# Optimization experiments

Measured on AMD Instinct MI355X. Metric: run time of the kernel, lower is better.

Reference implementation:

```python
import jax, jax.numpy as jnp
import numpy as np

# ---- static config (mirrors init_kwargs) ----
N_DIM = 3                      # manifold dimension n
D_COMP = 6                     # n(n+1)/2 metric components
M_PER = (12, 12, 12)           # HSGP basis functions per dim
M_STAR = 12 * 12 * 12          # 1728
T_STEPS = 50                   # time points in linspace(0,1,t)
C_SCALE = 1.5                  # HSGP domain scaling c
BATCH = 8192
ROWS = np.array([0, 1, 1, 2, 2, 2])   # lower-tri fill order of metric components
COLS = np.array([0, 0, 1, 0, 1, 2])


def _phi_dphi(x, L):
    """HSGP eigenfunctions and their spatial derivatives.
    x: [B, 3], L: [3] -> phi [B, M_STAR], dphi [B, M_STAR, 3]."""
    s, c = [], []
    for d in range(N_DIM):
        k = jnp.arange(1, M_PER[d] + 1, dtype=x.dtype)
        w = jnp.pi * k / (2.0 * L[d])                      # [m_d] frequencies
        arg = w[None, :] * (x[:, d:d + 1] + L[d])          # [B, m_d]
        scale = 1.0 / jnp.sqrt(L[d])
        s.append(scale * jnp.sin(arg))
        c.append(scale * jnp.cos(arg) * w[None, :])
    B = x.shape[0]
    phi = jnp.einsum('bi,bj,bk->bijk', s[0], s[1], s[2]).reshape(B, -1)
    d0 = jnp.einsum('bi,bj,bk->bijk', c[0], s[1], s[2]).reshape(B, -1)
    d1 = jnp.einsum('bi,bj,bk->bijk', s[0], c[1], s[2]).reshape(B, -1)
    d2 = jnp.einsum('bi,bj,bk->bijk', s[0], s[1], c[2]).reshape(B, -1)
    return phi, jnp.stack([d0, d1, d2], axis=-1)


def _omega(L):
    """[M_STAR, 3] angular frequencies of the tensor-product basis."""
    ks = [jnp.arange(1, m + 1, dtype=L.dtype) for m in M_PER]
    kg = jnp.stack(jnp.meshgrid(*ks, indexing='ij'), axis=-1).reshape(-1, N_DIM)
    return jnp.pi * kg / (2.0 * L[None, :])


def _metric_and_grad(x, W, L):
    """Metric g [B,3,3] and its spatial derivative dg [B,3,3,3] (last axis = d/dx_r)."""
    phi, dphi = _phi_dphi(x, L)
    gf = phi @ W.T                                   # [B, 6]
    dgf = jnp.einsum('bmr,dm->bdr', dphi, W)         # [B, 6, 3]
    B = x.shape[0]
    eye = jnp.eye(N_DIM, dtype=x.dtype)
    gl = jnp.zeros((B, N_DIM, N_DIM), x.dtype).at[:, ROWS, COLS].set(gf)
    g = gl + jnp.swapaxes(gl, 1, 2) - gl * eye + eye   # symmetrize + identity offset
    dgl = jnp.zeros((B, N_DIM, N_DIM, N_DIM), x.dtype).at[:, ROWS, COLS, :].set(dgf)
    dg = dgl + jnp.swapaxes(dgl, 1, 2) - dgl * eye[None, :, :, None]
    return g, dg


def _acceleration(pos, vel, W, L):
    """Geodesic equation: a^k = -Gamma^k_{ij} v^i v^j."""
    g, dg = _metric_and_grad(pos, W, L)
    ginv = jnp.linalg.inv(g)
    t1 = jnp.swapaxes(dg, 2, 3)            # [b,l,i,j] = d_i g_{lj}
    t3 = jnp.transpose(dg, (0, 3, 1, 2))   # [b,l,i,j] = d_l g_{ij}
    gamma = 0.5 * jnp.einsum('bkl,blij->bkij', ginv, t1 + dg - t3)
    return -jnp.einsum('bkij,bi,bj->bk', gamma, vel, vel)


def _integrate(pos0, vel0, W, L):
    dt = 1.0 / (T_STEPS - 1)

    def f(p, v):
        return v, _acceleration(p, v, W, L)

    def step(carry, _):
        p, v = carry
        dp1, dv1 = f(p, v)
        dp2, dv2 = f(p + 0.5 * dt * dp1, v + 0.5 * dt * dv1)
        dp3, dv3 = f(p + 0.5 * dt * dp2, v + 0.5 * dt * dv2)
        dp4, dv4 = f(p + dt * dp3, v + dt * dv3)
        pn = p + (dt / 6.0) * (dp1 + 2 * dp2 + 2 * dp3 + dp4)
        vn = v + (dt / 6.0) * (dv1 + 2 * dv2 + 2 * dv3 + dv4)
        return (pn, vn), (pn, vn)

    _, (ps, vs) = jax.lax.scan(step, (pos0, vel0), None, length=T_STEPS - 1)
    pos_traj = jnp.concatenate([pos0[None], ps], axis=0)   # [T, B, 3]
    vel_traj = jnp.concatenate([vel0[None], vs], axis=0)
    return jnp.stack([pos_traj, vel_traj], axis=1)          # [T, 2, B, 3]


def setup_inputs() -> dict:
    key = jax.random.key(0)
    k1, k2, k3, k4, k5 = jax.random.split(key, 5)
    return {
        'pos0': jax.random.normal(k1, (BATCH, N_DIM), jnp.float32),
        'vel0': jax.random.normal(k2, (BATCH, N_DIM), jnp.float32),
        'beta': 0.02 * jax.random.normal(k3, (D_COMP, M_STAR), jnp.float32),
        'ls': 0.5 + jax.random.uniform(k4, (D_COMP, N_DIM), jnp.float32),
        'basis': jax.random.normal(k5, (256, N_DIM), jnp.float32),
    }


def reference(pos0, vel0, beta, ls, basis):
    # HSGP domain half-widths from the linearization anchor points
    L = C_SCALE * jnp.max(jnp.abs(basis), axis=0)           # [3]
    om2 = _omega(L) ** 2                                     # [M_STAR, 3]
    # ExpQuad sqrt spectral density per GP component
    sqrt_psd = ((2.0 * jnp.pi) ** (N_DIM / 4.0)) \
        * jnp.sqrt(jnp.prod(ls, axis=1, keepdims=True)) \
        * jnp.exp(-0.25 * jnp.einsum('mi,di->dm', om2, ls ** 2))  # [6, M_STAR]
    W = beta * sqrt_psd                                      # [6, M_STAR]
    return _integrate(pos0, vel0, W, L)
```

## Files before the change

kernel.cpp:

```cpp
#include <hip/hip_runtime.h>
#include <math.h>

#define BATCH  8192
#define TSTEPS 50
#define PTS    32
#define NTHR   768
#define KSTR   168
#define GKSTR  160
#define TABSTR 100
#define NROW   96
#define PI_F   3.14159265358979323846f

typedef __bf16 bf16x8 __attribute__((ext_vector_type(8)));
typedef float  f32x4  __attribute__((ext_vector_type(4)));

__device__ __forceinline__ unsigned pack2bf(float a, float b) {
    unsigned short ua = __builtin_bit_cast(unsigned short, (__bf16)a);
    unsigned short ub = __builtin_bit_cast(unsigned short, (__bf16)b);
    return (unsigned)ua | ((unsigned)ub << 16);
}

__global__ void precompute_kernel(const float* __restrict__ beta,
                                  const float* __restrict__ ls,
                                  const float* __restrict__ basis,
                                  unsigned short* __restrict__ Wb,
                                  float* __restrict__ auxg)
{
    __shared__ float red[256];
    __shared__ float Ls[3], W1s[3];
    int t = threadIdx.x;

    for (int d = 0; d < 3; ++d) {
        red[t] = fabsf(basis[t*3 + d]);
        __syncthreads();
        for (int s = 128; s > 0; s >>= 1) {
            if (t < s) red[t] = fmaxf(red[t], red[t+s]);
            __syncthreads();
        }
        if (t == 0) {
            float L = 1.5f * red[0];
            Ls[d]  = L;
            W1s[d] = PI_F / (2.0f * L);
        }
        __syncthreads();
    }

    float pref[6], l20[6], l21[6], l22[6];
    #pragma unroll
    for (int dd = 0; dd < 6; ++dd) {
        float a = ls[dd*3+0], b = ls[dd*3+1], c = ls[dd*3+2];
        pref[dd] = 3.9685803f * sqrtf(a*b*c);
        l20[dd] = a*a; l21[dd] = b*b; l22[dd] = c*c;
    }

    for (int idx = t; idx < 96*GKSTR; idx += 256) {
        int n = idx / GKSTR, k = idx - n*GKSTR;
        int d = n >> 4, i = n & 15;
        float v = 0.0f;
        if (i < 12 && k < 144) {
            int j = k / 12, kk = k - (k/12)*12;
            float o0 = W1s[0]*(float)(i+1);
            float o1 = W1s[1]*(float)(j+1);
            float o2 = W1s[2]*(float)(kk+1);
            float e = expf(-0.25f*(o0*o0*l20[d] + o1*o1*l21[d] + o2*o2*l22[d]));
            v = beta[d*1728 + i*144 + k] * pref[d] * e;
        }
        Wb[idx] = __builtin_bit_cast(unsigned short, (__bf16)v);
    }

    if (t < 3) {
        auxg[t]     = Ls[t];
        auxg[3 + t] = W1s[t];
        auxg[6 + t] = 1.0f / sqrtf(Ls[t]);
    }
}

__global__ void __launch_bounds__(NTHR) geodesic_kernel(
    const float* __restrict__ pos0, const float* __restrict__ vel0,
    const unsigned short* __restrict__ Wbg, const float* __restrict__ auxg,
    float* __restrict__ out)
{
    __shared__ __align__(16) __bf16 P[NROW*KSTR];
    __shared__ __align__(16) float tabs[2][PTS][TABSTR];
    __shared__ __align__(16) float scr[2][PTS][28];

    const int tid = threadIdx.x;

    for (int idx = tid; idx < NROW*KSTR/2; idx += NTHR) ((unsigned*)P)[idx] = 0u;
    for (int idx = tid; idx < 2*PTS*TABSTR; idx += NTHR) ((float*)tabs)[idx] = 0.f;

    const float L0 = auxg[0], L1 = auxg[1], L2 = auxg[2];
    const float w10 = auxg[3], w11 = auxg[4], w12 = auxg[5];
    const float isq0 = auxg[6], isq1 = auxg[7], isq2 = auxg[8];

    const int w = tid >> 6, lane = tid & 63;
    const int nt = w >> 1, mb = (w & 1) * 3;
    const int lrow = lane & 15, lkg = lane >> 4;
    const int nn = nt*16 + lrow;
    const int ptn = nn / 3, pn = nn - 3*ptn;

    bf16x8 wfrag[3][5];
    {
        const __bf16* Wb = (const __bf16*)Wbg;
        #pragma unroll
        for (int mt = 0; mt < 3; ++mt)
            #pragma unroll
            for (int ks = 0; ks < 5; ++ks)
                wfrag[mt][ks] = *(const bf16x8*)(Wb + ((mb+mt)*16 + lrow)*GKSTR + ks*32 + lkg*8);
    }

    const bool owner = (w < 4);
    const int  myp = (w << 3) + (lane & 7);
    const int  rep = lane >> 3;
    float px=0,py=0,pz=0, vx=0,vy=0,vz=0, vcx=0,vcy=0,vcz=0;
    float vsx=0,vsy=0,vsz=0, asx=0,asy=0,asz=0;
    float pnx=0,pny=0,pnz=0;
    float qnx=0,qny=0,qnz=0;
    size_t pg3 = 0;

    const float dt  = 1.0f/49.0f;
    const float hdt = 0.5f/49.0f;
    const float sdt = dt/6.0f;

    if (owner) {
        pg3 = (size_t)(blockIdx.x * PTS + myp) * 3u;
        px = pos0[pg3+0]; py = pos0[pg3+1]; pz = pos0[pg3+2];
        vx = vel0[pg3+0]; vy = vel0[pg3+1]; vz = vel0[pg3+2];
        vcx = vx; vcy = vy; vcz = vz;
        qnx = fmaf(hdt,vx,px); qny = fmaf(hdt,vy,py); qnz = fmaf(hdt,vz,pz);
        if (lane < 8) {
            out[pg3+0] = px; out[pg3+1] = py; out[pg3+2] = pz;
            out[(size_t)BATCH*3 + pg3 + 0] = vx;
            out[(size_t)BATCH*3 + pg3 + 1] = vy;
            out[(size_t)BATCH*3 + pg3 + 2] = vz;
        }
    }
    __syncthreads();

    if (owner) {
        float* tp = &tabs[0][myp][0];
        #pragma unroll 1
        for (int r = rep; r < 36; r += 8) {
            int d = (r>=24)?2:((r>=12)?1:0);
            int k = r - 12*d;
            float q   = (d==0)?px:((d==1)?py:pz);
            float Ld  = (d==0)?L0:((d==1)?L1:L2);
            float w1d = (d==0)?w10:((d==1)?w11:w12);
            float isd = (d==0)?isq0:((d==1)?isq1:isq2);
            float wk = w1d * (float)(k+1);
            float sn, cs;
            __sincosf(wk*(q + Ld), &sn, &cs);
            int offs = (d==0)?0:((d==1)?32:56);
            int offc = offs + ((d==0)?16:12);
            tp[offs+k] = isd*sn;
            tp[offc+k] = isd*cs*wk;
        }
    }
    __syncthreads();

    #pragma unroll 1
    for (int g = 0; g <= 196; ++g) {
        const int cb = g & 1;

        if (g < 196 && !owner) {
            int idx = (w-4)*64 + lane;
            #pragma unroll 1
            for (int rr = 0; rr < 2; ++rr) {
                int u = idx + rr*512;
                if (rr == 1 && idx >= 256) break;
                int pt = u / 24;
                int role = u - pt*24;
                int j = role >> 1, kb = (role & 1)*6;
                const float* tb = &tabs[cb][pt][0];
                float s1 = tb[32 + j], c1 = tb[44 + j];
                float2 sa = *(const float2*)&tb[56 + kb];
                float2 sb = *(const float2*)&tb[58 + kb];
                float2 sg = *(const float2*)&tb[60 + kb];
                float2 ca = *(const float2*)&tb[68 + kb];
                float2 cbv = *(const float2*)&tb[70 + kb];
                float2 cg = *(const float2*)&tb[72 + kb];
                float s2v[6] = {sa.x, sa.y, sb.x, sb.y, sg.x, sg.y};
                float c2v[6] = {ca.x, ca.y, cbv.x, cbv.y, cg.x, cg.y};
                int colb = j*12 + kb;
                unsigned* pss = (unsigned*)&P[(pt*3 + 0)*KSTR + colb];
                unsigned* pcs = (unsigned*)&P[(pt*3 + 1)*KSTR + colb];
                unsigned* psc = (unsigned*)&P[(pt*3 + 2)*KSTR + colb];
                #pragma unroll
                for (int u2 = 0; u2 < 3; ++u2) {
                    pss[u2] = pack2bf(s1*s2v[2*u2], s1*s2v[2*u2+1]);
                    pcs[u2] = pack2bf(c1*s2v[2*u2], c1*s2v[2*u2+1]);
                    psc[u2] = pack2bf(s1*c2v[2*u2], s1*c2v[2*u2+1]);
                }
            }
        }
        if (g > 0 && owner) {
            const int sp = (g-1) & 3;
            const f32x4* spr = (const f32x4*)&scr[cb^1][myp][0];
            f32x4 q0 = spr[0], q1 = spr[1], q2 = spr[2], q3 = spr[3], q4 = spr[4], q5 = spr[5];

            float ux = vcx, uy = vcy, uz = vcz;

            float g00 = q0[0]+1.f, g10 = q0[1], g11 = q0[2]+1.f;
            float g20 = q0[3], g21 = q1[0], g22 = q1[1]+1.f;
            float d0a0=q1[2], d0a1=q1[3], d0a2=q2[0], d0a3=q2[1], d0a4=q2[2], d0a5=q2[3];
            float d1a0=q3[0], d1a1=q3[1], d1a2=q3[2], d1a3=q3[3], d1a4=q4[0], d1a5=q4[1];
            float d2a0=q4[2], d2a1=q4[3], d2a2=q5[0], d2a3=q5[1], d2a4=q5[2], d2a5=q5[3];

            float a00 = g11*g22 - g21*g21;
            float a01 = g20*g21 - g10*g22;
            float a02 = g10*g21 - g20*g11;
            float a11 = g00*g22 - g20*g20;
            float a12 = g10*g20 - g00*g21;
            float a22 = g00*g11 - g10*g10;
            float det = g00*a00 + g10*a01 + g20*a02;
            float inv = 1.0f / det;
            float h00=a00*inv, h01=a01*inv, h02=a02*inv;
            float h11=a11*inv, h12=a12*inv, h22=a22*inv;

            float t0 = ux*d0a0 + uy*d1a0 + uz*d2a0;
            float t1 = ux*d0a1 + uy*d1a1 + uz*d2a1;
            float t2 = ux*d0a2 + uy*d1a2 + uz*d2a2;
            float t3 = ux*d0a3 + uy*d1a3 + uz*d2a3;
            float t4 = ux*d0a4 + uy*d1a4 + uz*d2a4;
            float t5 = ux*d0a5 + uy*d1a5 + uz*d2a5;

            float hl0 = ux*t0 + uy*t1 + uz*t3;
            float hl1 = ux*t1 + uy*t2 + uz*t4;
            float hl2 = ux*t3 + uy*t4 + uz*t5;

            float xx = ux*ux, yy = uy*uy, zz = uz*uz;
            float xy2 = 2.f*ux*uy, xz2 = 2.f*ux*uz, yz2 = 2.f*uy*uz;
            float e0 = xx*d0a0 + xy2*d0a1 + yy*d0a2 + xz2*d0a3 + yz2*d0a4 + zz*d0a5;
            float e1 = xx*d1a0 + xy2*d1a1 + yy*d1a2 + xz2*d1a3 + yz2*d1a4 + zz*d1a5;
            float e2 = xx*d2a0 + xy2*d2a1 + yy*d2a2 + xz2*d2a3 + yz2*d2a4 + zz*d2a5;

            float C0 = hl0 - 0.5f*e0;
            float C1 = hl1 - 0.5f*e1;
            float C2 = hl2 - 0.5f*e2;
            float ax = -(h00*C0 + h01*C1 + h02*C2);
            float ay = -(h01*C0 + h11*C1 + h12*C2);
            float az = -(h02*C0 + h12*C1 + h22*C2);

            const float wgt = (sp == 1 || sp == 2) ? 2.f : 1.f;
            vsx += wgt*vcx; vsy += wgt*vcy; vsz += wgt*vcz;
            asx += wgt*ax;  asy += wgt*ay;  asz += wgt*az;

            if (sp == 0) {
                vcx = fmaf(hdt,ax,vx); vcy = fmaf(hdt,ay,vy); vcz = fmaf(hdt,az,vz);
                qnx = fmaf(hdt,vcx,px); qny = fmaf(hdt,vcy,py); qnz = fmaf(hdt,vcz,pz);
            } else if (sp == 1) {
                vcx = fmaf(hdt,ax,vx); vcy = fmaf(hdt,ay,vy); vcz = fmaf(hdt,az,vz);
                qnx = fmaf(dt,vcx,px); qny = fmaf(dt,vcy,py); qnz = fmaf(dt,vcz,pz);
            } else if (sp == 2) {
                vcx = fmaf(dt,ax,vx); vcy = fmaf(dt,ay,vy); vcz = fmaf(dt,az,vz);
                pnx = fmaf(sdt, vsx+vcx, px);
                pny = fmaf(sdt, vsy+vcy, py);
                pnz = fmaf(sdt, vsz+vcz, pz);
                qnx = pnx; qny = pny; qnz = pnz;
            } else {
                vx = fmaf(sdt, asx, vx); vy = fmaf(sdt, asy, vy); vz = fmaf(sdt, asz, vz);
                px = pnx; py = pny; pz = pnz;
                vcx = vx; vcy = vy; vcz = vz;
                qnx = fmaf(hdt,vx,px); qny = fmaf(hdt,vy,py); qnz = fmaf(hdt,vz,pz);
                vsx=vsy=vsz=0.f; asx=asy=asz=0.f;
                if (lane < 8) {
                    int step = (g-1) >> 2;
                    size_t ob = (size_t)(step+1) * 2u * BATCH * 3u;
                    out[ob + pg3 + 0] = px;
                    out[ob + pg3 + 1] = py;
                    out[ob + pg3 + 2] = pz;
                    out[ob + (size_t)BATCH*3 + pg3 + 0] = vx;
                    out[ob + (size_t)BATCH*3 + pg3 + 1] = vy;
                    out[ob + (size_t)BATCH*3 + pg3 + 2] = vz;
                }
            }
        }
        __syncthreads();

        if (g == 196) break;

        if (owner) {
            float* tp = &tabs[cb^1][myp][0];
            #pragma unroll 1
            for (int r = rep; r < 36; r += 8) {
                int d = (r>=24)?2:((r>=12)?1:0);
                int k = r - 12*d;
                float q   = (d==0)?qnx:((d==1)?qny:qnz);
                float Ld  = (d==0)?L0:((d==1)?L1:L2);
                float w1d = (d==0)?w10:((d==1)?w11:w12);
                float isd = (d==0)?isq0:((d==1)?isq1:isq2);
                float wk = w1d * (float)(k+1);
                float sn, cs;
                __sincosf(wk*(q + Ld), &sn, &cs);
                int offs = (d==0)?0:((d==1)?32:56);
                int offc = offs + ((d==0)?16:12);
                tp[offs+k] = isd*sn;
                tp[offc+k] = isd*cs*wk;
            }
        }
        {
            f32x4 acc0 = {0.f,0.f,0.f,0.f}, acc1 = {0.f,0.f,0.f,0.f}, acc2 = {0.f,0.f,0.f,0.f};
            #pragma unroll
            for (int ks = 0; ks < 5; ++ks) {
                bf16x8 pf = *(const bf16x8*)&P[nn*KSTR + ks*32 + lkg*8];
                acc0 = __builtin_amdgcn_mfma_f32_16x16x32_bf16(wfrag[0][ks], pf, acc0, 0, 0, 0);
                acc1 = __builtin_amdgcn_mfma_f32_16x16x32_bf16(wfrag[1][ks], pf, acc1, 0, 0, 0);
                acc2 = __builtin_amdgcn_mfma_f32_16x16x32_bf16(wfrag[2][ks], pf, acc2, 0, 0, 0);
            }

            f32x4 s0v = *(const f32x4*)&tabs[cb][ptn][lkg*4];
            f32x4 c0v = *(const f32x4*)&tabs[cb][ptn][16 + lkg*4];

            float vs0 = acc0[0]*s0v[0] + acc0[1]*s0v[1] + acc0[2]*s0v[2] + acc0[3]*s0v[3];
            float vs1 = acc1[0]*s0v[0] + acc1[1]*s0v[1] + acc1[2]*s0v[2] + acc1[3]*s0v[3];
            float vs2 = acc2[0]*s0v[0] + acc2[1]*s0v[1] + acc2[2]*s0v[2] + acc2[3]*s0v[3];
            float vc0 = acc0[0]*c0v[0] + acc0[1]*c0v[1] + acc0[2]*c0v[2] + acc0[3]*c0v[3];
            float vc1 = acc1[0]*c0v[0] + acc1[1]*c0v[1] + acc1[2]*c0v[2] + acc1[3]*c0v[3];
            float vc2 = acc2[0]*c0v[0] + acc2[1]*c0v[1] + acc2[2]*c0v[2] + acc2[3]*c0v[3];

            vs0 += __shfl_xor(vs0, 16); vs0 += __shfl_xor(vs0, 32);
            vs1 += __shfl_xor(vs1, 16); vs1 += __shfl_xor(vs1, 32);
            vs2 += __shfl_xor(vs2, 16); vs2 += __shfl_xor(vs2, 32);
            vc0 += __shfl_xor(vc0, 16); vc0 += __shfl_xor(vc0, 32);
            vc1 += __shfl_xor(vc1, 16); vc1 += __shfl_xor(vc1, 32);
            vc2 += __shfl_xor(vc2, 16); vc2 += __shfl_xor(vc2, 32);

            if (lkg == 0) {
                int off = (pn == 0) ? 0 : ((pn == 1) ? 12 : 18);
                scr[cb][ptn][off + mb + 0] = vs0;
                scr[cb][ptn][off + mb + 1] = vs1;
                scr[cb][ptn][off + mb + 2] = vs2;
            }
            if (lkg == 1 && pn == 0) {
                scr[cb][ptn][6 + mb + 0] = vc0;
                scr[cb][ptn][6 + mb + 1] = vc1;
                scr[cb][ptn][6 + mb + 2] = vc2;
            }
        }
        __syncthreads();
    }
}

extern "C" void kernel_launch(void* const* d_in, const int* in_sizes, int n_in,
                              void* d_out, int out_size, void* d_ws, size_t ws_size,
                              hipStream_t stream) {
    (void)in_sizes; (void)n_in; (void)out_size; (void)ws_size;
    const float* pos0  = (const float*)d_in[0];
    const float* vel0  = (const float*)d_in[1];
    const float* beta  = (const float*)d_in[2];
    const float* ls    = (const float*)d_in[3];
    const float* basis = (const float*)d_in[4];
    float* outp = (float*)d_out;

    unsigned short* Wb = (unsigned short*)d_ws;
    float* auxg = (float*)((char*)d_ws + 96*GKSTR*sizeof(unsigned short));

    precompute_kernel<<<1, 256, 0, stream>>>(beta, ls, basis, Wb, auxg);
    geodesic_kernel<<<BATCH/PTS, NTHR, 0, stream>>>(pos0, vel0, Wb, auxg, outp);
}
```

Before: 418.7 us.

## Redistribute next-step sin/cos table computation from owner lanes to non-owner waves

Owner lanes now publish the next query positions to a small shared array, and the sin/cos table for the following step is built by the non-owner waves, spread over all 1152 point-entry pairs. Previously only the 8 replicated lanes per point did this work serially alongside their integration role. The intent is to balance work across waves and overlap table generation with the owners' MFMA work. The cost is an extra shared-memory handoff that depends on the existing barrier, and the non-owner waves take on more per-step work.

```diff
diff --git a/kernel.cpp b/kernel.cpp
--- a/kernel.cpp
+++ b/kernel.cpp
@@ -8,6 +8,7 @@
 #define KSTR   168
 #define GKSTR  160
 #define TABSTR 100
+#define QSTR   5
 #define NROW   96
 #define PI_F   3.14159265358979323846f
 
@@ -18,6 +19,12 @@
     unsigned short ua = __builtin_bit_cast(unsigned short, (__bf16)a);
     unsigned short ub = __builtin_bit_cast(unsigned short, (__bf16)b);
     return (unsigned)ua | ((unsigned)ub << 16);
+}
+
+__device__ __forceinline__ float bfly_add(float v) {
+    v += __shfl_xor(v, 16);
+    v += __shfl_xor(v, 32);
+    return v;
 }
 
 __global__ void precompute_kernel(const float* __restrict__ beta,
@@ -83,6 +90,7 @@
     __shared__ __align__(16) __bf16 P[NROW*KSTR];
     __shared__ __align__(16) float tabs[2][PTS][TABSTR];
     __shared__ __align__(16) float scr[2][PTS][28];
+    __shared__ float qs[PTS][QSTR];
 
     const int tid = threadIdx.x;
 
@@ -129,6 +137,7 @@
         vcx = vx; vcy = vy; vcz = vz;
         qnx = fmaf(hdt,vx,px); qny = fmaf(hdt,vy,py); qnz = fmaf(hdt,vz,pz);
         if (lane < 8) {
+            qs[myp][0] = qnx; qs[myp][1] = qny; qs[myp][2] = qnz;
             out[pg3+0] = px; out[pg3+1] = py; out[pg3+2] = pz;
             out[(size_t)BATCH*3 + pg3 + 0] = vx;
             out[(size_t)BATCH*3 + pg3 + 1] = vy;
@@ -274,18 +283,23 @@
                     out[ob + (size_t)BATCH*3 + pg3 + 2] = vz;
                 }
             }
+            if (lane < 8) {
+                qs[myp][0] = qnx; qs[myp][1] = qny; qs[myp][2] = qnz;
+            }
         }
         __syncthreads();
 
         if (g == 196) break;
 
-        if (owner) {
-            float* tp = &tabs[cb^1][myp][0];
+        if (!owner) {
+            int base = (w-4)*64 + lane;
             #pragma unroll 1
-            for (int r = rep; r < 36; r += 8) {
-                int d = (r>=24)?2:((r>=12)?1:0);
-                int k = r - 12*d;
-                float q   = (d==0)?qnx:((d==1)?qny:qnz);
+            for (int u = base; u < 1152; u += 512) {
+                int pt = u / 36;
+                int r  = u - 36*pt;
+                int d  = (r>=24)?2:((r>=12)?1:0);
+                int k  = r - 12*d;
+                float q   = qs[pt][d];
                 float Ld  = (d==0)?L0:((d==1)?L1:L2);
                 float w1d = (d==0)?w10:((d==1)?w11:w12);
                 float isd = (d==0)?isq0:((d==1)?isq1:isq2);
@@ -294,8 +308,8 @@
                 __sincosf(wk*(q + Ld), &sn, &cs);
                 int offs = (d==0)?0:((d==1)?32:56);
                 int offc = offs + ((d==0)?16:12);
-                tp[offs+k] = isd*sn;
-                tp[offc+k] = isd*cs*wk;
+                tabs[cb^1][pt][offs+k] = isd*sn;
+                tabs[cb^1][pt][offc+k] = isd*cs*wk;
             }
         }
         {
@@ -318,12 +332,8 @@
             float vc1 = acc1[0]*c0v[0] + acc1[1]*c0v[1] + acc1[2]*c0v[2] + acc1[3]*c0v[3];
             float vc2 = acc2[0]*c0v[0] + acc2[1]*c0v[1] + acc2[2]*c0v[2] + acc2[3]*c0v[3];
 
-            vs0 += __shfl_xor(vs0, 16); vs0 += __shfl_xor(vs0, 32);
-            vs1 += __shfl_xor(vs1, 16); vs1 += __shfl_xor(vs1, 32);
-            vs2 += __shfl_xor(vs2, 16); vs2 += __shfl_xor(vs2, 32);
-            vc0 += __shfl_xor(vc0, 16); vc0 += __shfl_xor(vc0, 32);
-            vc1 += __shfl_xor(vc1, 16); vc1 += __shfl_xor(vc1, 32);
-            vc2 += __shfl_xor(vc2, 16); vc2 += __shfl_xor(vc2, 32);
+            vs0 = bfly_add(vs0); vs1 = bfly_add(vs1); vs2 = bfly_add(vs2);
+            vc0 = bfly_add(vc0); vc1 = bfly_add(vc1); vc2 = bfly_add(vc2);
 
             if (lkg == 0) {
                 int off = (pn == 0) ? 0 : ((pn == 1) ? 12 : 18);
```

Result: slower. 427.6 us (+2.1%).

## Specialize waves: 12 GEMM waves build P and run MFMA, 4 owner waves integrate

Applied to the files above, without the earlier changes.

Raises the block from 768 to 1024 threads and splits the waves into roles. Waves 0-11 now both build the bf16 basis matrix P (one entry per thread, with no second pass) and run the MFMA products. Waves 12-15 handle only the ODE integration and the sin/cos tables, no longer doing MFMA work as well. The aim is to shorten the serial work per grid step by letting the owner and GEMM work run on separate waves. The cost is more registers and scheduling pressure per CU from the larger block.

```diff
diff --git a/kernel.cpp b/kernel.cpp
--- a/kernel.cpp
+++ b/kernel.cpp
@@ -4,7 +4,7 @@
 #define BATCH  8192
 #define TSTEPS 50
 #define PTS    32
-#define NTHR   768
+#define NTHR   1024
 #define KSTR   168
 #define GKSTR  160
 #define TABSTR 100
@@ -18,6 +18,12 @@
     unsigned short ua = __builtin_bit_cast(unsigned short, (__bf16)a);
     unsigned short ub = __builtin_bit_cast(unsigned short, (__bf16)b);
     return (unsigned)ua | ((unsigned)ub << 16);
+}
+
+__device__ __forceinline__ float bfly_add(float v) {
+    v += __shfl_xor(v, 16);
+    v += __shfl_xor(v, 32);
+    return v;
 }
 
 __global__ void precompute_kernel(const float* __restrict__ beta,
@@ -94,13 +100,14 @@
     const float isq0 = auxg[6], isq1 = auxg[7], isq2 = auxg[8];
 
     const int w = tid >> 6, lane = tid & 63;
+    const bool gemm_wave = (w < 12);
     const int nt = w >> 1, mb = (w & 1) * 3;
     const int lrow = lane & 15, lkg = lane >> 4;
     const int nn = nt*16 + lrow;
     const int ptn = nn / 3, pn = nn - 3*ptn;
 
     bf16x8 wfrag[3][5];
-    {
+    if (gemm_wave) {
         const __bf16* Wb = (const __bf16*)Wbg;
         #pragma unroll
         for (int mt = 0; mt < 3; ++mt)
@@ -109,8 +116,8 @@
                 wfrag[mt][ks] = *(const bf16x8*)(Wb + ((mb+mt)*16 + lrow)*GKSTR + ks*32 + lkg*8);
     }
 
-    const bool owner = (w < 4);
-    const int  myp = (w << 3) + (lane & 7);
+    const bool owner = (w >= 12);
+    const int  myp = ((w - 12) << 3) + (lane & 7);
     const int  rep = lane >> 3;
     float px=0,py=0,pz=0, vx=0,vy=0,vz=0, vcx=0,vcy=0,vcz=0;
     float vsx=0,vsy=0,vsz=0, asx=0,asy=0,asz=0;
@@ -162,35 +169,30 @@
     for (int g = 0; g <= 196; ++g) {
         const int cb = g & 1;
 
-        if (g < 196 && !owner) {
-            int idx = (w-4)*64 + lane;
-            #pragma unroll 1
-            for (int rr = 0; rr < 2; ++rr) {
-                int u = idx + rr*512;
-                if (rr == 1 && idx >= 256) break;
-                int pt = u / 24;
-                int role = u - pt*24;
-                int j = role >> 1, kb = (role & 1)*6;
-                const float* tb = &tabs[cb][pt][0];
-                float s1 = tb[32 + j], c1 = tb[44 + j];
-                float2 sa = *(const float2*)&tb[56 + kb];
-                float2 sb = *(const float2*)&tb[58 + kb];
-                float2 sg = *(const float2*)&tb[60 + kb];
-                float2 ca = *(const float2*)&tb[68 + kb];
-                float2 cbv = *(const float2*)&tb[70 + kb];
-                float2 cg = *(const float2*)&tb[72 + kb];
-                float s2v[6] = {sa.x, sa.y, sb.x, sb.y, sg.x, sg.y};
-                float c2v[6] = {ca.x, ca.y, cbv.x, cbv.y, cg.x, cg.y};
-                int colb = j*12 + kb;
-                unsigned* pss = (unsigned*)&P[(pt*3 + 0)*KSTR + colb];
-                unsigned* pcs = (unsigned*)&P[(pt*3 + 1)*KSTR + colb];
-                unsigned* psc = (unsigned*)&P[(pt*3 + 2)*KSTR + colb];
-                #pragma unroll
-                for (int u2 = 0; u2 < 3; ++u2) {
-                    pss[u2] = pack2bf(s1*s2v[2*u2], s1*s2v[2*u2+1]);
-                    pcs[u2] = pack2bf(c1*s2v[2*u2], c1*s2v[2*u2+1]);
-                    psc[u2] = pack2bf(s1*c2v[2*u2], s1*c2v[2*u2+1]);
-                }
+        if (g < 196 && gemm_wave) {
+            int u = tid;
+            int pt = u / 24;
+            int role = u - pt*24;
+            int j = role >> 1, kb = (role & 1)*6;
+            const float* tb = &tabs[cb][pt][0];
+            float s1 = tb[32 + j], c1 = tb[44 + j];
+            float2 sa = *(const float2*)&tb[56 + kb];
+            float2 sb = *(const float2*)&tb[58 + kb];
+            float2 sg = *(const float2*)&tb[60 + kb];
+            float2 ca = *(const float2*)&tb[68 + kb];
+            float2 cbv = *(const float2*)&tb[70 + kb];
+            float2 cg = *(const float2*)&tb[72 + kb];
+            float s2v[6] = {sa.x, sa.y, sb.x, sb.y, sg.x, sg.y};
+            float c2v[6] = {ca.x, ca.y, cbv.x, cbv.y, cg.x, cg.y};
+            int colb = j*12 + kb;
+            unsigned* pss = (unsigned*)&P[(pt*3 + 0)*KSTR + colb];
+            unsigned* pcs = (unsigned*)&P[(pt*3 + 1)*KSTR + colb];
+            unsigned* psc = (unsigned*)&P[(pt*3 + 2)*KSTR + colb];
+            #pragma unroll
+            for (int u2 = 0; u2 < 3; ++u2) {
+                pss[u2] = pack2bf(s1*s2v[2*u2], s1*s2v[2*u2+1]);
+                pcs[u2] = pack2bf(c1*s2v[2*u2], c1*s2v[2*u2+1]);
+                psc[u2] = pack2bf(s1*c2v[2*u2], s1*c2v[2*u2+1]);
             }
         }
         if (g > 0 && owner) {
@@ -297,8 +299,7 @@
                 tp[offs+k] = isd*sn;
                 tp[offc+k] = isd*cs*wk;
             }
-        }
-        {
+        } else {
             f32x4 acc0 = {0.f,0.f,0.f,0.f}, acc1 = {0.f,0.f,0.f,0.f}, acc2 = {0.f,0.f,0.f,0.f};
             #pragma unroll
             for (int ks = 0; ks < 5; ++ks) {
@@ -318,12 +319,8 @@
             float vc1 = acc1[0]*c0v[0] + acc1[1]*c0v[1] + acc1[2]*c0v[2] + acc1[3]*c0v[3];
             float vc2 = acc2[0]*c0v[0] + acc2[1]*c0v[1] + acc2[2]*c0v[2] + acc2[3]*c0v[3];
 
-            vs0 += __shfl_xor(vs0, 16); vs0 += __shfl_xor(vs0, 32);
-            vs1 += __shfl_xor(vs1, 16); vs1 += __shfl_xor(vs1, 32);
-            vs2 += __shfl_xor(vs2, 16); vs2 += __shfl_xor(vs2, 32);
-            vc0 += __shfl_xor(vc0, 16); vc0 += __shfl_xor(vc0, 32);
-            vc1 += __shfl_xor(vc1, 16); vc1 += __shfl_xor(vc1, 32);
-            vc2 += __shfl_xor(vc2, 16); vc2 += __shfl_xor(vc2, 32);
+            vs0 = bfly_add(vs0); vs1 = bfly_add(vs1); vs2 = bfly_add(vs2);
+            vc0 = bfly_add(vc0); vc1 = bfly_add(vc1); vc2 = bfly_add(vc2);
 
             if (lkg == 0) {
                 int off = (pn == 0) ? 0 : ((pn == 1) ? 12 : 18);
```

New measurement: 412.6 us (median of 2 runs). No clear change (-1.4%).
